# Kernel tuning notes

Measured on AMD Instinct MI355X. Metric: run time of the kernel, lower is better.

## Reference

```python
import jax, jax.numpy as jnp
import numpy as np


def _sqdist(emb):
    # emb: (B, F, N) -> pairwise squared euclidean distance over feature dim: (B, N, N)
    g = jnp.einsum('bfi,bfj->bij', emb, emb)
    sq = jnp.sum(emb * emb, axis=1)  # (B, N)
    return sq[:, :, None] + sq[:, None, :] - 2.0 * g


def _forward(emb, alpha, beta):
    B, F, N = emb.shape
    sqdist = _sqdist(emb)                        # (B, N, N)
    momentum = emb[:, 4, :]                      # (B, N)
    # pow_momenta = exp(2*alpha*log(p)) == p ** (2*alpha)
    pow_momenta = jnp.exp(2.0 * alpha * jnp.log(momentum))   # (B, N)
    # sym_min: m_ij = min(p_i, p_j)
    min_momenta = jnp.minimum(pow_momenta[:, :, None], pow_momenta[:, None, :])
    d_ij = sqdist * min_momenta                  # (B, N, N)
    # _renorm: mask diagonal with a huge value, subtract/divide by global per-tensor min
    eye = jnp.eye(N, dtype=d_ij.dtype)
    big = 1000.0 * jax.lax.stop_gradient(jnp.max(d_ij))
    d_nodiag = d_ij + big * eye[None, :, :]
    # original: min over dim 1 then dim 2 (keepdim semantics) -> per-batch scalar min
    d_min = jnp.min(d_nodiag, axis=(1, 2), keepdims=True)    # (B, 1, 1)
    d_center = (d_nodiag - d_min) / d_min
    d_norm = -(beta ** 2) * d_center             # beta (1,1,1) broadcasts
    # softmax over rows (last dim), applied per (node-row) after flattening batch
    return jax.nn.softmax(d_norm, axis=-1)


def setup_inputs() -> dict:
    key = jax.random.key(0)
    k1, = jax.random.split(key, 1)
    B, F, N = 32, 6, 1024
    emb = jax.random.uniform(k1, (B, F, N), dtype=jnp.float32, minval=0.01, maxval=1.0)
    alpha = jnp.ones((1, 1), dtype=jnp.float32)
    beta = jnp.ones((1, 1, 1), dtype=jnp.float32)
    return {"emb": emb, "alpha": alpha, "beta": beta}


def reference(emb, alpha, beta):
    return _forward(emb, alpha, beta)
```

## Files before the change

### kernel.cpp

```cpp
#include <hip/hip_runtime.h>
#include <math.h>

#define BB 32
#define FF 6
#define NN 1024

typedef float f4 __attribute__((ext_vector_type(4)));

template <int CTRL, int RMASK>
__device__ __forceinline__ float dpp_f(float v, float old) {
    return __builtin_bit_cast(float,
        __builtin_amdgcn_update_dpp(__builtin_bit_cast(int, old),
                                    __builtin_bit_cast(int, v),
                                    CTRL, RMASK, 0xF, false));
}
__device__ __forceinline__ float wave_min64(float v) {
    const float I = __builtin_inff();
    v = fminf(v, dpp_f<0x111, 0xF>(v, I));
    v = fminf(v, dpp_f<0x112, 0xF>(v, I));
    v = fminf(v, dpp_f<0x114, 0xF>(v, I));
    v = fminf(v, dpp_f<0x118, 0xF>(v, I));
    v = fminf(v, dpp_f<0x142, 0xA>(v, I));
    v = fminf(v, dpp_f<0x143, 0xC>(v, I));
    return __builtin_bit_cast(float,
        __builtin_amdgcn_readlane(__builtin_bit_cast(int, v), 63));
}
__device__ __forceinline__ float wave_sum64(float v) {
    v += dpp_f<0x111, 0xF>(v, 0.0f);
    v += dpp_f<0x112, 0xF>(v, 0.0f);
    v += dpp_f<0x114, 0xF>(v, 0.0f);
    v += dpp_f<0x118, 0xF>(v, 0.0f);
    v += dpp_f<0x142, 0xA>(v, 0.0f);
    v += dpp_f<0x143, 0xC>(v, 0.0f);
    return __builtin_bit_cast(float,
        __builtin_amdgcn_readlane(__builtin_bit_cast(int, v), 63));
}

__device__ __forceinline__ float4 pm4(float4 m, float a2) {
    float4 r;
    if (a2 == 2.0f) {
        r.x = m.x * m.x; r.y = m.y * m.y; r.z = m.z * m.z; r.w = m.w * m.w;
    } else {
        r.x = expf(a2 * logf(m.x));
        r.y = expf(a2 * logf(m.y));
        r.z = expf(a2 * logf(m.z));
        r.w = expf(a2 * logf(m.w));
    }
    return r;
}

__global__ __launch_bounds__(256) void k_min(const float* __restrict__ emb,
                                             const float* __restrict__ alphap,
                                             float* __restrict__ partial) {
    __shared__ float s_tile[7][NN];
    __shared__ float red[4];
    const int b = blockIdx.x >> 5, chunk = blockIdx.x & 31;
    const int tid = threadIdx.x, wid = tid >> 6, lane = tid & 63;
    const float* e = emb + (size_t)b * FF * NN;

    #pragma unroll
    for (int t = 0; t < 6; ++t) {
        const int idx = t * 256 + tid;
        const int f = idx >> 8, j4 = idx & 255;
        ((float4*)&s_tile[f][0])[j4] = ((const float4*)(e + (size_t)f * NN))[j4];
    }
    {
        const float a2 = 2.0f * alphap[0];
        float4 m = *(const float4*)(e + 4 * NN + 4 * tid);
        *(float4*)&s_tile[6][4 * tid] = pm4(m, a2);
    }
    __syncthreads();

    float vmin = 3.4e38f;
    #pragma unroll
    for (int g = 0; g < 2; ++g) {
        int ii[4];
        float ei[4][FF], pmi[4];
        #pragma unroll
        for (int rr = 0; rr < 4; ++rr) {
            ii[rr] = chunk + 32 * wid + 128 * (g * 4 + rr);
            #pragma unroll
            for (int f = 0; f < FF; ++f) ei[rr][f] = s_tile[f][ii[rr]];
            pmi[rr] = s_tile[6][ii[rr]];
        }
        #pragma unroll
        for (int k = 0; k < 4; ++k) {
            if (k >= (ii[0] >> 8)) {
                float4 q[FF], pk4;
                #pragma unroll
                for (int f = 0; f < FF; ++f)
                    q[f] = ((const float4*)&s_tile[f][k * 256])[lane];
                pk4 = ((const float4*)&s_tile[6][k * 256])[lane];
                #pragma unroll
                for (int rr = 0; rr < 4; ++rr) {
                    const int i = ii[rr], km = i >> 8;
                    if (k > km) {
                        #pragma unroll
                        for (int c = 0; c < 4; ++c) {
                            float acc = 0.0f;
                            #pragma unroll
                            for (int f = 0; f < FF; ++f) {
                                float t = ((const float*)&q[f])[c] - ei[rr][f];
                                acc = fmaf(t, t, acc);
                            }
                            vmin = fminf(vmin,
                                acc * fminf(pmi[rr], ((const float*)&pk4)[c]));
                        }
                    } else if (k == km) {
                        #pragma unroll
                        for (int c = 0; c < 4; ++c) {
                            float acc = 0.0f;
                            #pragma unroll
                            for (int f = 0; f < FF; ++f) {
                                float t = ((const float*)&q[f])[c] - ei[rr][f];
                                acc = fmaf(t, t, acc);
                            }
                            float dd = acc * fminf(pmi[rr], ((const float*)&pk4)[c]);
                            const int j = k * 256 + lane * 4 + c;
                            vmin = (j > i) ? fminf(vmin, dd) : vmin;
                        }
                    }
                }
            }
        }
    }
    vmin = wave_min64(vmin);
    if (lane == 0) red[wid] = vmin;
    __syncthreads();
    if (tid == 0)
        partial[blockIdx.x] = fminf(fminf(red[0], red[1]), fminf(red[2], red[3]));
}

__global__ __launch_bounds__(256) void k_soft(const float* __restrict__ emb,
                                              const float* __restrict__ alphap,
                                              const float* __restrict__ betap,
                                              const float* __restrict__ partial,
                                              float* __restrict__ out) {
    __shared__ float s_tile[7][NN];
    __shared__ float s_dmin;
    const int b = blockIdx.x >> 5, chunk = blockIdx.x & 31;
    const int tid = threadIdx.x, wid = tid >> 6, lane = tid & 63;
    const float* e = emb + (size_t)b * FF * NN;

    if (tid < 32) {
        float v = partial[b * 32 + tid];
        #pragma unroll
        for (int o = 16; o >= 1; o >>= 1) v = fminf(v, __shfl_xor(v, o));
        if (tid == 0) s_dmin = v;
    }
    #pragma unroll
    for (int t = 0; t < 6; ++t) {
        const int idx = t * 256 + tid;
        const int f = idx >> 8, j4 = idx & 255;
        ((float4*)&s_tile[f][0])[j4] = ((const float4*)(e + (size_t)f * NN))[j4];
    }
    __syncthreads();
    const float beta = betap[0];
    const float s2 = beta * beta / s_dmin * 1.4426950408889634f;
    {
        const float a2 = 2.0f * alphap[0];
        float4 m = *(const float4*)(e + 4 * NN + 4 * tid);
        float4 r = pm4(m, a2);
        r.x *= s2; r.y *= s2; r.z *= s2; r.w *= s2;
        *(float4*)&s_tile[6][4 * tid] = r;
    }
    __syncthreads();

    const int kd = chunk >> 3;
    #pragma unroll
    for (int g = 0; g < 2; ++g) {
        int ii[4];
        float ei[4][FF], pmi[4];
        #pragma unroll
        for (int rr = 0; rr < 4; ++rr) {
            ii[rr] = chunk * 32 + wid * 8 + g * 4 + rr;
            #pragma unroll
            for (int f = 0; f < FF; ++f) ei[rr][f] = s_tile[f][ii[rr]];
            pmi[rr] = s_tile[6][ii[rr]];
        }
        float d[4][16];
        #pragma unroll
        for (int k = 0; k < 4; ++k) {
            float4 q[FF], pk4;
            #pragma unroll
            for (int f = 0; f < FF; ++f)
                q[f] = ((const float4*)&s_tile[f][k * 256])[lane];
            pk4 = ((const float4*)&s_tile[6][k * 256])[lane];
            #pragma unroll
            for (int rr = 0; rr < 4; ++rr) {
                #pragma unroll
                for (int c = 0; c < 4; ++c) {
                    float acc = 0.0f;
                    #pragma unroll
                    for (int f = 0; f < FF; ++f) {
                        float t = ((const float*)&q[f])[c] - ei[rr][f];
                        acc = fmaf(t, t, acc);
                    }
                    d[rr][k * 4 + c] =
                        acc * fminf(pmi[rr], ((const float*)&pk4)[c]);
                }
            }
            if (k == kd) {
                #pragma unroll
                for (int rr = 0; rr < 4; ++rr) {
                    #pragma unroll
                    for (int c = 0; c < 4; ++c)
                        if (k * 256 + lane * 4 + c == ii[rr])
                            d[rr][k * 4 + c] = __builtin_inff();
                }
            }
        }
        #pragma unroll
        for (int rr = 0; rr < 4; ++rr) {
            float rmin = fminf(d[rr][0], d[rr][1]);
            #pragma unroll
            for (int t = 2; t < 16; ++t) rmin = fminf(rmin, d[rr][t]);
            rmin = wave_min64(rmin);

            float sum = 0.0f;
            #pragma unroll
            for (int t = 0; t < 16; ++t) {
                float p = __builtin_amdgcn_exp2f(rmin - d[rr][t]);
                d[rr][t] = p;
                sum += p;
            }
            sum = wave_sum64(sum);
            const float inv = 1.0f / sum;

            float* op = out + ((size_t)b * NN + (size_t)ii[rr]) * NN;
            #pragma unroll
            for (int k = 0; k < 4; ++k) {
                f4 w;
                w.x = d[rr][k * 4 + 0] * inv;
                w.y = d[rr][k * 4 + 1] * inv;
                w.z = d[rr][k * 4 + 2] * inv;
                w.w = d[rr][k * 4 + 3] * inv;
                __builtin_nontemporal_store(w, (f4*)&op[k * 256 + lane * 4]);
            }
        }
    }
}

extern "C" void kernel_launch(void* const* d_in, const int* in_sizes, int n_in,
                              void* d_out, int out_size, void* d_ws, size_t ws_size,
                              hipStream_t stream) {
    const float* emb   = (const float*)d_in[0];
    const float* alpha = (const float*)d_in[1];
    const float* beta  = (const float*)d_in[2];
    float* out = (float*)d_out;
    float* partial = (float*)d_ws;

    k_min <<<BB * 32, 256, 0, stream>>>(emb, alpha, partial);
    k_soft<<<BB * 32, 256, 0, stream>>>(emb, alpha, beta, partial, out);
}
```

Measured before the change: 39.38 us.

## Assign contiguous row blocks per chunk and load only needed columns in k_min

Rows are now assigned to blocks contiguously (chunk*32 + wid*8 + r), so each block's rows lie in a single 256-column segment km. Each block then loads into shared memory only columns from km onward instead of the full tile, cutting global loads and pow computations for the triangular min. The trade-off is load imbalance across blocks: blocks with km=0 process all four segments while km=3 blocks process one. The loop also handles one row at a time instead of four, which lowers register pressure but gives less ILP and reuse of the q loads.

```diff
diff --git a/kernel.cpp b/kernel.cpp
--- a/kernel.cpp
+++ b/kernel.cpp
@@ -57,68 +57,66 @@
     const int b = blockIdx.x >> 5, chunk = blockIdx.x & 31;
     const int tid = threadIdx.x, wid = tid >> 6, lane = tid & 63;
     const float* e = emb + (size_t)b * FF * NN;
+    const int km = chunk >> 3;
+    const int nst = (4 - km) * 64;
 
     #pragma unroll
-    for (int t = 0; t < 6; ++t) {
-        const int idx = t * 256 + tid;
-        const int f = idx >> 8, j4 = idx & 255;
-        ((float4*)&s_tile[f][0])[j4] = ((const float4*)(e + (size_t)f * NN))[j4];
+    for (int f = 0; f < FF; ++f) {
+        if (tid < nst) {
+            const int j4 = km * 64 + tid;
+            ((float4*)&s_tile[f][0])[j4] =
+                ((const float4*)(e + (size_t)f * NN))[j4];
+        }
     }
     {
         const float a2 = 2.0f * alphap[0];
-        float4 m = *(const float4*)(e + 4 * NN + 4 * tid);
-        *(float4*)&s_tile[6][4 * tid] = pm4(m, a2);
+        if (tid < nst) {
+            const int j4 = km * 64 + tid;
+            float4 m = ((const float4*)(e + 4 * NN))[j4];
+            ((float4*)&s_tile[6][0])[j4] = pm4(m, a2);
+        }
     }
     __syncthreads();
 
     float vmin = 3.4e38f;
-    #pragma unroll
-    for (int g = 0; g < 2; ++g) {
-        int ii[4];
-        float ei[4][FF], pmi[4];
-        #pragma unroll
-        for (int rr = 0; rr < 4; ++rr) {
-            ii[rr] = chunk + 32 * wid + 128 * (g * 4 + rr);
-            #pragma unroll
-            for (int f = 0; f < FF; ++f) ei[rr][f] = s_tile[f][ii[rr]];
-            pmi[rr] = s_tile[6][ii[rr]];
-        }
+    for (int r = 0; r < 8; ++r) {
+        const int i = chunk * 32 + wid * 8 + r;
+        float eif[FF];
+        #pragma unroll
+        for (int f = 0; f < FF; ++f) eif[f] = s_tile[f][i];
+        const float pmi = s_tile[6][i];
         #pragma unroll
         for (int k = 0; k < 4; ++k) {
-            if (k >= (ii[0] >> 8)) {
+            if (k >= km) {
                 float4 q[FF], pk4;
                 #pragma unroll
                 for (int f = 0; f < FF; ++f)
                     q[f] = ((const float4*)&s_tile[f][k * 256])[lane];
                 pk4 = ((const float4*)&s_tile[6][k * 256])[lane];
-                #pragma unroll
-                for (int rr = 0; rr < 4; ++rr) {
-                    const int i = ii[rr], km = i >> 8;
-                    if (k > km) {
+                if (k > km) {
+                    #pragma unroll
+                    for (int c = 0; c < 4; ++c) {
+                        float acc = 0.0f;
                         #pragma unroll
-                        for (int c = 0; c < 4; ++c) {
-                            float acc = 0.0f;
-                            #pragma unroll
-                            for (int f = 0; f < FF; ++f) {
-                                float t = ((const float*)&q[f])[c] - ei[rr][f];
-                                acc = fmaf(t, t, acc);
-                            }
-                            vmin = fminf(vmin,
-                                acc * fminf(pmi[rr], ((const float*)&pk4)[c]));
+                        for (int f = 0; f < FF; ++f) {
+                            float t = ((const float*)&q[f])[c] - eif[f];
+                            acc = fmaf(t, t, acc);
                         }
-                    } else if (k == km) {
+                        vmin = fminf(vmin,
+                            acc * fminf(pmi, ((const float*)&pk4)[c]));
+                    }
+                } else {
+                    #pragma unroll
+                    for (int c = 0; c < 4; ++c) {
+                        float acc = 0.0f;
                         #pragma unroll
-                        for (int c = 0; c < 4; ++c) {
-                            float acc = 0.0f;
-                            #pragma unroll
-                            for (int f = 0; f < FF; ++f) {
-                                float t = ((const float*)&q[f])[c] - ei[rr][f];
-                                acc = fmaf(t, t, acc);
-                            }
-                            float dd = acc * fminf(pmi[rr], ((const float*)&pk4)[c]);
-                            const int j = k * 256 + lane * 4 + c;
-                            vmin = (j > i) ? fminf(vmin, dd) : vmin;
+                        for (int f = 0; f < FF; ++f) {
+                            float t = ((const float*)&q[f])[c] - eif[f];
+                            acc = fmaf(t, t, acc);
                         }
+                        float dd = acc * fminf(pmi, ((const float*)&pk4)[c]);
+                        const int j = k * 256 + lane * 4 + c;
+                        vmin = (j > i) ? fminf(vmin, dd) : vmin;
                     }
                 }
             }
```

New measurement: 42.90 us. +8.9%, slower.
